# Optimization experiments

Measured on AMD Instinct MI355X. Metric: run time of the kernel, lower is better.

Reference implementation:

```python
import jax, jax.numpy as jnp
import numpy as np

B, L, DM, H, DK, DV, DH = 16, 1024, 512, 8, 64, 64, 2048
FACTOR = 5
EPS = 1e-5


def _ln(x, g, b):
    m = x.mean(-1, keepdims=True)
    v = jnp.mean((x - m) ** 2, axis=-1, keepdims=True)
    return g * (x - m) / jnp.sqrt(v + EPS) + b


def setup_inputs() -> dict:
    key = jax.random.key(0)
    ks = jax.random.split(key, 12)
    w = lambda k, s: jax.random.normal(k, s, jnp.float32) * 0.02
    sample_k = min(FACTOR * int(np.ceil(np.log(L))), L)  # 35
    return {
        "x": jax.random.normal(ks[0], (B, L, DM), jnp.float32),
        "Wq": w(ks[1], (DM, H * DK)), "bq": jnp.zeros((H * DK,), jnp.float32),
        "Wk": w(ks[2], (DM, H * DK)), "bk": jnp.zeros((H * DK,), jnp.float32),
        "Wv": w(ks[3], (DM, H * DV)), "bv": jnp.zeros((H * DV,), jnp.float32),
        "Wo": w(ks[4], (H * DV, DM)), "bo": jnp.zeros((DM,), jnp.float32),
        "g1": jnp.ones((DM,), jnp.float32), "beta1": jnp.zeros((DM,), jnp.float32),
        "W1": w(ks[5], (DM, DH)), "bf1": jnp.zeros((DH,), jnp.float32),
        "W2": w(ks[6], (DH, DM)), "bf2": jnp.zeros((DM,), jnp.float32),
        "g2": jnp.ones((DM,), jnp.float32), "beta2": jnp.zeros((DM,), jnp.float32),
        "index_sample": jax.random.randint(ks[7], (L, sample_k), 0, L),
        "stage": 0,  # eval; mask=False so attn_mask is always False
    }


def _prob_attention(Q, K, V, index_sample):
    # Q,K,V: [B,H,L,D] (Informer ProbAttention, mask_flag=False, eval)
    Bq, Hq, Lq, D = Q.shape
    u = index_sample.shape[1]  # u == U_part since L_Q == L_K
    # sparse sampled scores: K gathered per-query -> [B,H,L,sample_k,D]
    K_sample = K[:, :, index_sample, :]
    QK_sample = jnp.einsum("bhld,bhlsd->bhls", Q, K_sample)
    M = QK_sample.max(-1) - QK_sample.mean(-1)            # [B,H,L] sparsity measure
    _, M_top = jax.lax.top_k(M, u)                         # [B,H,u]
    Q_reduce = jnp.take_along_axis(Q, M_top[..., None], axis=2)  # [B,H,u,D]
    scores = jnp.einsum("bhud,bhld->bhul", Q_reduce, K) / jnp.sqrt(jnp.float32(D))
    attn = jax.nn.softmax(scores, axis=-1)                 # [B,H,u,L]
    # initial context = mean of V over keys, broadcast to all queries
    context = jnp.broadcast_to(V.mean(axis=2, keepdims=True), V.shape)
    bi = jnp.arange(Bq)[:, None, None]
    hi = jnp.arange(Hq)[None, :, None]
    context = context.at[bi, hi, M_top].set(jnp.einsum("bhul,bhld->bhud", attn, V))
    # output_attention=True: uniform 1/L everywhere, true attn at selected queries
    attns = jnp.full((Bq, Hq, Lq, Lq), 1.0 / Lq, dtype=attn.dtype)
    attns = attns.at[bi, hi, M_top].set(attn)
    return context, attns


def reference(x, Wq, bq, Wk, bk, Wv, bv, Wo, bo, g1, beta1, W1, bf1, W2, bf2, g2, beta2, index_sample, stage):
    residual = x
    Q = (x @ Wq + bq).reshape(B, L, H, DK).transpose(0, 2, 1, 3)
    K = (x @ Wk + bk).reshape(B, L, H, DK).transpose(0, 2, 1, 3)
    V = (x @ Wv + bv).reshape(B, L, H, DV).transpose(0, 2, 1, 3)
    ctx, score = _prob_attention(Q, K, V, index_sample)
    ctx = ctx.transpose(0, 2, 1, 3).reshape(B, L, H * DV)
    out = ctx @ Wo + bo
    x1 = _ln(out + residual, g1, beta1)          # dropout = identity (eval)
    ffn = jax.nn.relu(x1 @ W1 + bf1) @ W2 + bf2
    x2 = _ln(ffn + x1, g2, beta2)
    return x2, score
```

## Files before the change

### kernel.cpp

```cpp
#include <hip/hip_runtime.h>
#include <cstdint>
#include <cstddef>

#define Bc 16
#define Lc 1024
#define DMc 512
#define Hc 8
#define DHc 2048
#define Uc 35

typedef __attribute__((ext_vector_type(8))) short bf16x8;
typedef __attribute__((ext_vector_type(4))) float f32x4;

__device__ __forceinline__ ushort f2bf(float f) {
    union { float f; uint32_t u; } v; v.f = f;
    uint32_t r = v.u + 0x7FFF + ((v.u >> 16) & 1);
    return (ushort)(r >> 16);
}
__device__ __forceinline__ float bf2f(ushort u) {
    union { uint32_t i; float f; } v; v.i = ((uint32_t)u) << 16; return v.f;
}

__device__ __forceinline__ void glds16(const ushort* g, ushort* l) {
    __builtin_amdgcn_global_load_lds(
        (__attribute__((address_space(1))) void*)(void*)const_cast<ushort*>(g),
        (__attribute__((address_space(3))) void*)l, 16, 0, 0);
}

template<int MODE>
__global__ __launch_bounds__(256) void gemm_mfma(
    const ushort* __restrict__ A, const ushort* __restrict__ Bt,
    const float* __restrict__ bias, void* __restrict__ out0,
    void* __restrict__ out1, int M, int N, int K, int nxb)
{
    __shared__ ushort As[128 * 64];
    __shared__ ushort Bs[128 * 64];
    const int nwg = gridDim.x;
    int wg = blockIdx.x;
    wg = (wg & 7) * (nwg >> 3) + (wg >> 3);
    const int n0 = (wg % nxb) * 128;
    const int m0 = (wg / nxb) * 128;

    const int tid = threadIdx.x;
    const int lane = tid & 63;
    const int wave = tid >> 6;
    const int wr = wave >> 1, wc = wave & 1;
    const int lrow = lane & 15;
    const int lk = (lane >> 4) * 8;

    f32x4 zero = {0.f, 0.f, 0.f, 0.f};
    f32x4 acc[4][4];
    #pragma unroll
    for (int m = 0; m < 4; ++m)
        #pragma unroll
        for (int n = 0; n < 4; ++n) acc[m][n] = zero;

    const int srow = tid >> 3;
    const int skc = (tid & 7) * 8;
    const int ldsb = (tid & 192) * 8;

    for (int k0 = 0; k0 < K; k0 += 64) {
        #pragma unroll
        for (int r = 0; r < 4; ++r) {
            glds16(A  + (size_t)(m0 + r * 32 + srow) * K + k0 + skc, &As[r * 2048 + ldsb]);
            glds16(Bt + (size_t)(n0 + r * 32 + srow) * K + k0 + skc, &Bs[r * 2048 + ldsb]);
        }
        __syncthreads();
        #pragma unroll
        for (int kk = 0; kk < 2; ++kk) {
            bf16x8 af[4], bv[4];
            #pragma unroll
            for (int m = 0; m < 4; ++m)
                af[m] = *reinterpret_cast<const bf16x8*>(&As[(wr * 64 + m * 16 + lrow) * 64 + kk * 32 + lk]);
            #pragma unroll
            for (int n = 0; n < 4; ++n)
                bv[n] = *reinterpret_cast<const bf16x8*>(&Bs[(wc * 64 + n * 16 + lrow) * 64 + kk * 32 + lk]);
            #pragma unroll
            for (int m = 0; m < 4; ++m)
                #pragma unroll
                for (int n = 0; n < 4; ++n)
                    acc[m][n] = __builtin_amdgcn_mfma_f32_16x16x32_bf16(af[m], bv[n], acc[m][n], 0, 0, 0);
        }
        __syncthreads();
    }

    #pragma unroll
    for (int n = 0; n < 4; ++n) {
        int col = n0 + wc * 64 + n * 16 + lrow;
        float bval = bias[col];
        #pragma unroll
        for (int m = 0; m < 4; ++m) {
            #pragma unroll
            for (int j = 0; j < 4; ++j) {
                int row = m0 + wr * 64 + m * 16 + (lane >> 4) * 4 + j;
                float v = acc[m][n][j] + bval;
                if (MODE == 2) v = fmaxf(v, 0.0f);
                if (MODE == 0)
                    ((float*)out0)[(size_t)row * N + col] = v;
                else if (MODE == 1 || MODE == 2)
                    ((ushort*)out0)[(size_t)row * N + col] = f2bf(v);
                else {
                    if (col < 1024) ((ushort*)out0)[(size_t)row * 1024 + col] = f2bf(v);
                    else            ((float*)out1)[(size_t)row * 512 + (col - 1024)] = v;
                }
            }
        }
    }
}

__device__ __forceinline__ void tr_tile(
    const float* __restrict__ in, ushort* __restrict__ out,
    int K, int N, int bx, int by, float (*t)[33], int tid)
{
    int n0 = bx * 32, k0 = by * 32;
    int tx = tid & 31, ty = tid >> 5;
    #pragma unroll
    for (int dy = 0; dy < 32; dy += 8)
        t[ty + dy][tx] = in[(size_t)(k0 + ty + dy) * N + n0 + tx];
    __syncthreads();
    #pragma unroll
    for (int dy = 0; dy < 32; dy += 8)
        out[(size_t)(n0 + ty + dy) * K + k0 + tx] = f2bf(t[tx][ty + dy]);
}

__global__ __launch_bounds__(256) void prep_kernel(
    const float* __restrict__ x,
    const float* __restrict__ Wq, const float* __restrict__ Wk,
    const float* __restrict__ Wv, const float* __restrict__ Wo,
    const float* __restrict__ W1, const float* __restrict__ W2,
    const float* __restrict__ bq, const float* __restrict__ bk,
    const float* __restrict__ bv,
    ushort* __restrict__ xbf, ushort* __restrict__ Wqkvt,
    ushort* __restrict__ Wot, ushort* __restrict__ W1t,
    ushort* __restrict__ W2t, float* __restrict__ bcat)
{
    __shared__ float t[32][33];
    const int tid = threadIdx.x;
    int bid = blockIdx.x;
    if (bid < 8192) {
        int i = bid * 256 + tid;
        float4 v = reinterpret_cast<const float4*>(x)[i];
        uint32_t lo = (uint32_t)f2bf(v.x) | ((uint32_t)f2bf(v.y) << 16);
        uint32_t hi = (uint32_t)f2bf(v.z) | ((uint32_t)f2bf(v.w) << 16);
        reinterpret_cast<uint2*>(xbf)[i] = make_uint2(lo, hi);
        return;
    }
    bid -= 8192;
    if (bid < 256) { tr_tile(Wq, Wqkvt,              512, 512, bid & 15, bid >> 4, t, tid); return; }
    bid -= 256;
    if (bid < 256) { tr_tile(Wk, Wqkvt + 512 * 512,  512, 512, bid & 15, bid >> 4, t, tid); return; }
    bid -= 256;
    if (bid < 256) { tr_tile(Wv, Wqkvt + 1024 * 512, 512, 512, bid & 15, bid >> 4, t, tid); return; }
    bid -= 256;
    if (bid < 256) { tr_tile(Wo, Wot,                512, 512, bid & 15, bid >> 4, t, tid); return; }
    bid -= 256;
    if (bid < 1024) { tr_tile(W1, W1t,               512, 2048, bid & 63, bid >> 6, t, tid); return; }
    bid -= 1024;
    if (bid < 1024) { tr_tile(W2, W2t,               2048, 512, bid & 15, bid >> 4, t, tid); return; }
    for (int i = tid; i < 1536; i += 256)
        bcat[i] = (i < 512) ? bq[i] : (i < 1024) ? bk[i - 512] : bv[i - 1024];
}

__global__ __launch_bounds__(256) void fill_score_kernel(float* __restrict__ s)
{
    const float iv = 1.0f / (float)Lc;
    float4 v = make_float4(iv, iv, iv, iv);
    size_t i = (size_t)blockIdx.x * 256 + threadIdx.x;
    const size_t nthreads = (size_t)32768 * 256;
    float4* p = reinterpret_cast<float4*>(s);
    #pragma unroll
    for (int c = 0; c < 4; ++c) p[i + c * nthreads] = v;
}

__global__ __launch_bounds__(256) void compute_M_kernel(
    const ushort* __restrict__ QK, const int* __restrict__ idx,
    float* __restrict__ Mout)
{
    __shared__ float qs[4][64];
    const int tid = threadIdx.x;
    const int wid = tid >> 6;
    const int lane = tid & 63;
    const int task = blockIdx.x * 4 + wid;
    const int l = task & (Lc - 1);
    const int bh = task >> 10;
    const int h = bh & (Hc - 1);
    const int b = bh >> 3;

    qs[wid][lane] = bf2f(QK[(size_t)(b * Lc + l) * 1024 + h * 64 + lane]);

    const bool act = lane < Uc;
    int kl = act ? idx[l * Uc + lane] : 0;
    const bf16x8* kr = reinterpret_cast<const bf16x8*>(
        QK + (size_t)(b * Lc + kl) * 1024 + 512 + h * 64);
    float dot = 0.0f;
    if (act) {
        #pragma unroll
        for (int c = 0; c < 8; ++c) {
            bf16x8 kv = kr[c];
            #pragma unroll
            for (int e = 0; e < 8; ++e)
                dot += qs[wid][c * 8 + e] * bf2f((ushort)kv[e]);
        }
    }
    float mx = act ? dot : -INFINITY;
    float sm = act ? dot : 0.0f;
    #pragma unroll
    for (int off = 32; off; off >>= 1) {
        mx = fmaxf(mx, __shfl_xor(mx, off, 64));
        sm += __shfl_xor(sm, off, 64);
    }
    if (lane == 0) Mout[task] = mx - sm * (1.0f / Uc);
}

__global__ __launch_bounds__(256) void topk_kernel(
    const float* __restrict__ Mvals, int* __restrict__ Mtop)
{
    int bh = blockIdx.x;
    __shared__ float vals[Lc];
    __shared__ float rv[256];
    __shared__ int   ri[256];
    int t = threadIdx.x;
    for (int i = t; i < Lc; i += 256)
        vals[i] = Mvals[(size_t)bh * Lc + i];
    __syncthreads();
    for (int j = 0; j < Uc; ++j) {
        float bv = -INFINITY; int bi = Lc;
        for (int i = t; i < Lc; i += 256) {
            float v = vals[i];
            if (v > bv) { bv = v; bi = i; }
        }
        rv[t] = bv; ri[t] = bi;
        __syncthreads();
        for (int s = 128; s; s >>= 1) {
            if (t < s) {
                float v2 = rv[t + s]; int i2 = ri[t + s];
                if (v2 > rv[t] || (v2 == rv[t] && i2 < ri[t])) { rv[t] = v2; ri[t] = i2; }
            }
            __syncthreads();
        }
        if (t == 0) {
            int bidx = ri[0];
            Mtop[bh * Uc + j] = bidx;
            vals[bidx] = -INFINITY;
        }
        __syncthreads();
    }
}

__global__ __launch_bounds__(256) void qk_scores_kernel(
    const ushort* __restrict__ QK, const int* __restrict__ Mtop,
    float* __restrict__ score)
{
    const int bh = blockIdx.x >> 2;
    const int l0 = (blockIdx.x & 3) * 256;
    const int h = bh & (Hc - 1), b = bh >> 3;
    __shared__ int qpos[Uc];
    __shared__ float Qs[Uc][64];
    const int t = threadIdx.x;
    if (t < Uc) qpos[t] = Mtop[bh * Uc + t];
    __syncthreads();
    for (int i = t; i < Uc * 64; i += 256) {
        int j = i >> 6, d = i & 63;
        Qs[j][d] = bf2f(QK[(size_t)(b * Lc + qpos[j]) * 1024 + h * 64 + d]);
    }
    __syncthreads();

    const int l = l0 + t;
    const bf16x8* kr = reinterpret_cast<const bf16x8*>(
        QK + (size_t)(b * Lc + l) * 1024 + 512 + h * 64);
    float acc[Uc] = {};
    #pragma unroll
    for (int c = 0; c < 8; ++c) {
        bf16x8 kv = kr[c];
        float kf[8];
        #pragma unroll
        for (int e = 0; e < 8; ++e) kf[e] = bf2f((ushort)kv[e]);
        #pragma unroll
        for (int j = 0; j < Uc; ++j) {
            float s = 0.0f;
            #pragma unroll
            for (int e = 0; e < 8; ++e) s += Qs[j][c * 8 + e] * kf[e];
            acc[j] += s;
        }
    }
    #pragma unroll
    for (int j = 0; j < Uc; ++j)
        score[((size_t)(bh << 10) + qpos[j]) * Lc + l] = acc[j] * 0.125f;
}

__global__ __launch_bounds__(256) void attn_out_kernel(
    float* __restrict__ score, const float* __restrict__ V,
    const int* __restrict__ Mtop, ushort* __restrict__ ctx)
{
    const int bh = blockIdx.x;
    const int h = bh & (Hc - 1), b = bh >> 3;
    const int t = threadIdx.x;
    const int d = t & 63, part = t >> 6;

    __shared__ int qpos[Uc];
    __shared__ float mz[Uc][2];
    __shared__ float buf[4][Uc][64];
    __shared__ float vmred[4][64];
    __shared__ float vmf[64];

    if (t < Uc) qpos[t] = Mtop[bh * Uc + t];
    __syncthreads();

    for (int j = part; j < Uc; j += 4) {
        const float* row = score + ((size_t)(bh << 10) + qpos[j]) * Lc;
        float v[16];
        float mx = -INFINITY;
        #pragma unroll
        for (int c = 0; c < 16; ++c) { v[c] = row[c * 64 + d]; mx = fmaxf(mx, v[c]); }
        #pragma unroll
        for (int off = 32; off; off >>= 1) mx = fmaxf(mx, __shfl_xor(mx, off, 64));
        float z = 0.0f;
        #pragma unroll
        for (int c = 0; c < 16; ++c) z += expf(v[c] - mx);
        #pragma unroll
        for (int off = 32; off; off >>= 1) z += __shfl_xor(z, off, 64);
        if (d == 0) { mz[j][0] = mx; mz[j][1] = 1.0f / z; }
    }
    __syncthreads();

    float acc[Uc];
    #pragma unroll
    for (int j = 0; j < Uc; ++j) acc[j] = 0.0f;
    float vm = 0.0f;

    for (int c = 0; c < 4; ++c) {
        const int l0 = part * 256 + c * 64;
        #pragma unroll
        for (int j = 0; j < Uc; ++j) {
            size_t off = ((size_t)(bh << 10) + qpos[j]) * Lc + l0 + d;
            float p = expf(score[off] - mz[j][0]) * mz[j][1];
            buf[part][j][d] = p;
            score[off] = p;
        }
        __syncthreads();
        #pragma unroll 4
        for (int li = 0; li < 64; ++li) {
            float v = V[((size_t)(b << 10) + l0 + li) * 512 + h * 64 + d];
            vm += v;
            #pragma unroll
            for (int j = 0; j < Uc; ++j) acc[j] += buf[part][j][li] * v;
        }
        __syncthreads();
    }

    #pragma unroll
    for (int j = 0; j < Uc; ++j) buf[part][j][d] = acc[j];
    vmred[part][d] = vm;
    __syncthreads();
    if (t < 64) vmf[t] = (vmred[0][t] + vmred[1][t] + vmred[2][t] + vmred[3][t]) * (1.0f / Lc);
    __syncthreads();

    const int dcol = (t & 15) * 4;
    ushort4 vmu;
    vmu.x = f2bf(vmf[dcol + 0]); vmu.y = f2bf(vmf[dcol + 1]);
    vmu.z = f2bf(vmf[dcol + 2]); vmu.w = f2bf(vmf[dcol + 3]);
    for (int li = 0; li < 64; ++li) {
        int l = (t >> 4) + li * 16;
        *reinterpret_cast<ushort4*>(ctx + ((size_t)(b << 10) + l) * 512 + h * 64 + dcol) = vmu;
    }
    __syncthreads();

    for (int idx = t; idx < Uc * 64; idx += 256) {
        int j = idx >> 6, d2 = idx & 63;
        float s = buf[0][j][d2] + buf[1][j][d2] + buf[2][j][d2] + buf[3][j][d2];
        ctx[((size_t)(b << 10) + qpos[j]) * 512 + h * 64 + d2] = f2bf(s);
    }
}

template<int A_BF, int B_BF, int OUT_BF>
__global__ __launch_bounds__(256) void ln_kernel(
    const void* __restrict__ a, const void* __restrict__ bsrc,
    const float* __restrict__ g, const float* __restrict__ beta,
    void* __restrict__ y)
{
    const int row = blockIdx.x;
    const int t = threadIdx.x;
    float a0, a1, b0, b1;
    if (A_BF) {
        uint32_t u = ((const uint32_t*)a)[(size_t)row * 256 + t];
        a0 = bf2f((ushort)(u & 0xffff)); a1 = bf2f((ushort)(u >> 16));
    } else {
        float2 f = ((const float2*)a)[(size_t)row * 256 + t];
        a0 = f.x; a1 = f.y;
    }
    if (B_BF) {
        uint32_t u = ((const uint32_t*)bsrc)[(size_t)row * 256 + t];
        b0 = bf2f((ushort)(u & 0xffff)); b1 = bf2f((ushort)(u >> 16));
    } else {
        float2 f = ((const float2*)bsrc)[(size_t)row * 256 + t];
        b0 = f.x; b1 = f.y;
    }
    float v0 = a0 + b0, v1 = a1 + b1;
    __shared__ float red[256];
    red[t] = v0 + v1; __syncthreads();
    for (int s = 128; s; s >>= 1) { if (t < s) red[t] += red[t + s]; __syncthreads(); }
    float mean = red[0] * (1.0f / DMc);
    __syncthreads();
    float d0 = v0 - mean, d1 = v1 - mean;
    red[t] = d0 * d0 + d1 * d1; __syncthreads();
    for (int s = 128; s; s >>= 1) { if (t < s) red[t] += red[t + s]; __syncthreads(); }
    float inv = rsqrtf(red[0] * (1.0f / DMc) + 1e-5f);
    float2 gv = ((const float2*)g)[t];
    float2 bt = ((const float2*)beta)[t];
    float o0 = gv.x * d0 * inv + bt.x;
    float o1 = gv.y * d1 * inv + bt.y;
    if (OUT_BF) {
        uint32_t u = (uint32_t)f2bf(o0) | ((uint32_t)f2bf(o1) << 16);
        ((uint32_t*)y)[(size_t)row * 256 + t] = u;
    } else {
        ((float2*)y)[(size_t)row * 256 + t] = make_float2(o0, o1);
    }
}

extern "C" void kernel_launch(void* const* d_in, const int* in_sizes, int n_in,
                              void* d_out, int out_size, void* d_ws, size_t ws_size,
                              hipStream_t stream)
{
    const float* x     = (const float*)d_in[0];
    const float* Wq    = (const float*)d_in[1];
    const float* bq    = (const float*)d_in[2];
    const float* Wk    = (const float*)d_in[3];
    const float* bk    = (const float*)d_in[4];
    const float* Wv    = (const float*)d_in[5];
    const float* bv    = (const float*)d_in[6];
    const float* Wo    = (const float*)d_in[7];
    const float* bo    = (const float*)d_in[8];
    const float* g1    = (const float*)d_in[9];
    const float* beta1 = (const float*)d_in[10];
    const float* W1    = (const float*)d_in[11];
    const float* bf1   = (const float*)d_in[12];
    const float* W2    = (const float*)d_in[13];
    const float* bf2   = (const float*)d_in[14];
    const float* g2    = (const float*)d_in[15];
    const float* beta2 = (const float*)d_in[16];
    const int* index_sample = (const int*)d_in[17];

    const size_t NTOK = (size_t)Bc * Lc;
    const size_t QKV_SZ = NTOK * DMc;
    const size_t HID_SZ = NTOK * DHc;

    char* p = (char*)d_ws;
    auto alloc = [&](size_t bytes) { char* r = p; p += (bytes + 255) & ~(size_t)255; return r; };
    ushort* QKbf   = (ushort*)alloc(NTOK * 1024 * 2);
    float*  V      = (float*) alloc(QKV_SZ * 4);
    ushort* hidden = (ushort*)alloc(HID_SZ * 2);
    ushort* xbf    = (ushort*)alloc(QKV_SZ * 2);
    ushort* ctxbf  = (ushort*)alloc(QKV_SZ * 2);
    ushort* x1bf   = (ushort*)alloc(QKV_SZ * 2);
    ushort* projbf = (ushort*)alloc(QKV_SZ * 2);
    float*  ffnf   = (float*) alloc(QKV_SZ * 4);
    ushort* Wqkvt  = (ushort*)alloc((size_t)1536 * 512 * 2);
    ushort* Wot    = (ushort*)alloc((size_t)512 * 512 * 2);
    ushort* W1t    = (ushort*)alloc((size_t)512 * 2048 * 2);
    ushort* W2t    = (ushort*)alloc((size_t)512 * 2048 * 2);
    float*  bcat   = (float*) alloc(1536 * 4);
    float*  Mbuf   = (float*) alloc((size_t)Bc * Hc * Lc * 4);
    int*    Mtop   = (int*)   alloc((size_t)Bc * Hc * 64 * 4);

    float* x2_out    = (float*)d_out;
    float* score_out = x2_out + QKV_SZ;

    dim3 blk(256);

    fill_score_kernel<<<32768, blk, 0, stream>>>(score_out);
    prep_kernel<<<8192 + 4 * 256 + 2 * 1024 + 1, blk, 0, stream>>>(
        x, Wq, Wk, Wv, Wo, W1, W2, bq, bk, bv,
        xbf, Wqkvt, Wot, W1t, W2t, bcat);

    gemm_mfma<3><<<12 * 128, blk, 0, stream>>>(
        xbf, Wqkvt, bcat, QKbf, V, (int)NTOK, 1536, 512, 12);

    compute_M_kernel<<<(Bc * Hc * Lc) / 4, blk, 0, stream>>>(QKbf, index_sample, Mbuf);
    topk_kernel<<<Bc * Hc, blk, 0, stream>>>(Mbuf, Mtop);

    qk_scores_kernel<<<Bc * Hc * 4, blk, 0, stream>>>(QKbf, Mtop, score_out);
    attn_out_kernel<<<Bc * Hc, blk, 0, stream>>>(score_out, V, Mtop, ctxbf);

    gemm_mfma<1><<<4 * 128, blk, 0, stream>>>(
        ctxbf, Wot, bo, projbf, nullptr, (int)NTOK, 512, 512, 4);
    ln_kernel<1, 0, 1><<<(int)NTOK, blk, 0, stream>>>(projbf, x, g1, beta1, x1bf);

    gemm_mfma<2><<<16 * 128, blk, 0, stream>>>(
        x1bf, W1t, bf1, hidden, nullptr, (int)NTOK, 2048, 512, 16);
    gemm_mfma<0><<<4 * 128, blk, 0, stream>>>(
        hidden, W2t, bf2, ffnf, nullptr, (int)NTOK, 512, 2048, 4);
    ln_kernel<0, 1, 0><<<(int)NTOK, blk, 0, stream>>>(ffnf, x1bf, g2, beta2, x2_out);
}
```

Measured before the change: 665.0 us.

## Double-buffer GEMM LDS tiles, merge score fill into prep, warp-shuffle top-k

The GEMM now uses two LDS buffers and issues the next K tile's global-to-LDS loads before computing on the current tile, which removes one barrier per iteration and overlaps loads with MFMA. The uniform score fill is merged into the prep kernel to save a launch. Top-k keeps the M values in registers and does the argmax with wave shuffles plus a 4-way final step, replacing the many-barrier LDS tree. Doubling LDS per GEMM block may reduce occupancy.

Result: no change. 667.6 us (+0.4%).

```diff
diff --git a/kernel.cpp b/kernel.cpp
--- a/kernel.cpp
+++ b/kernel.cpp
@@ -33,8 +33,8 @@
     const float* __restrict__ bias, void* __restrict__ out0,
     void* __restrict__ out1, int M, int N, int K, int nxb)
 {
-    __shared__ ushort As[128 * 64];
-    __shared__ ushort Bs[128 * 64];
+    __shared__ ushort As[2][128 * 64];
+    __shared__ ushort Bs[2][128 * 64];
     const int nwg = gridDim.x;
     int wg = blockIdx.x;
     wg = (wg & 7) * (nwg >> 3) + (wg >> 3);
@@ -59,22 +59,29 @@
     const int skc = (tid & 7) * 8;
     const int ldsb = (tid & 192) * 8;
 
-    for (int k0 = 0; k0 < K; k0 += 64) {
+    auto stage = [&](int k0, int bufi) {
         #pragma unroll
         for (int r = 0; r < 4; ++r) {
-            glds16(A  + (size_t)(m0 + r * 32 + srow) * K + k0 + skc, &As[r * 2048 + ldsb]);
-            glds16(Bt + (size_t)(n0 + r * 32 + srow) * K + k0 + skc, &Bs[r * 2048 + ldsb]);
-        }
-        __syncthreads();
+            glds16(A  + (size_t)(m0 + r * 32 + srow) * K + k0 + skc, &As[bufi][r * 2048 + ldsb]);
+            glds16(Bt + (size_t)(n0 + r * 32 + srow) * K + k0 + skc, &Bs[bufi][r * 2048 + ldsb]);
+        }
+    };
+
+    const int nt = K >> 6;
+    stage(0, 0);
+    __syncthreads();
+    int cur = 0;
+    for (int t = 0; t < nt; ++t) {
+        if (t + 1 < nt) stage((t + 1) << 6, cur ^ 1);
         #pragma unroll
         for (int kk = 0; kk < 2; ++kk) {
             bf16x8 af[4], bv[4];
             #pragma unroll
             for (int m = 0; m < 4; ++m)
-                af[m] = *reinterpret_cast<const bf16x8*>(&As[(wr * 64 + m * 16 + lrow) * 64 + kk * 32 + lk]);
+                af[m] = *reinterpret_cast<const bf16x8*>(&As[cur][(wr * 64 + m * 16 + lrow) * 64 + kk * 32 + lk]);
             #pragma unroll
             for (int n = 0; n < 4; ++n)
-                bv[n] = *reinterpret_cast<const bf16x8*>(&Bs[(wc * 64 + n * 16 + lrow) * 64 + kk * 32 + lk]);
+                bv[n] = *reinterpret_cast<const bf16x8*>(&Bs[cur][(wc * 64 + n * 16 + lrow) * 64 + kk * 32 + lk]);
             #pragma unroll
             for (int m = 0; m < 4; ++m)
                 #pragma unroll
@@ -82,6 +89,7 @@
                     acc[m][n] = __builtin_amdgcn_mfma_f32_16x16x32_bf16(af[m], bv[n], acc[m][n], 0, 0, 0);
         }
         __syncthreads();
+        cur ^= 1;
     }
 
     #pragma unroll
@@ -123,6 +131,9 @@
         out[(size_t)(n0 + ty + dy) * K + k0 + tx] = f2bf(t[tx][ty + dy]);
 }
 
+#define PREP_BLKS (8192 + 4 * 256 + 2 * 1024 + 1)
+#define FILL_BLKS 32768
+
 __global__ __launch_bounds__(256) void prep_kernel(
     const float* __restrict__ x,
     const float* __restrict__ Wq, const float* __restrict__ Wk,
@@ -132,7 +143,8 @@
     const float* __restrict__ bv,
     ushort* __restrict__ xbf, ushort* __restrict__ Wqkvt,
     ushort* __restrict__ Wot, ushort* __restrict__ W1t,
-    ushort* __restrict__ W2t, float* __restrict__ bcat)
+    ushort* __restrict__ W2t, float* __restrict__ bcat,
+    float* __restrict__ score_out)
 {
     __shared__ float t[32][33];
     const int tid = threadIdx.x;
@@ -157,17 +169,18 @@
     if (bid < 1024) { tr_tile(W1, W1t,               512, 2048, bid & 63, bid >> 6, t, tid); return; }
     bid -= 1024;
     if (bid < 1024) { tr_tile(W2, W2t,               2048, 512, bid & 15, bid >> 4, t, tid); return; }
-    for (int i = tid; i < 1536; i += 256)
-        bcat[i] = (i < 512) ? bq[i] : (i < 1024) ? bk[i - 512] : bv[i - 1024];
-}
-
-__global__ __launch_bounds__(256) void fill_score_kernel(float* __restrict__ s)
-{
+    bid -= 1024;
+    if (bid < 1) {
+        for (int i = tid; i < 1536; i += 256)
+            bcat[i] = (i < 512) ? bq[i] : (i < 1024) ? bk[i - 512] : bv[i - 1024];
+        return;
+    }
+    bid -= 1;
     const float iv = 1.0f / (float)Lc;
     float4 v = make_float4(iv, iv, iv, iv);
-    size_t i = (size_t)blockIdx.x * 256 + threadIdx.x;
-    const size_t nthreads = (size_t)32768 * 256;
-    float4* p = reinterpret_cast<float4*>(s);
+    size_t i = (size_t)bid * 256 + tid;
+    const size_t nthreads = (size_t)FILL_BLKS * 256;
+    float4* p = reinterpret_cast<float4*>(score_out);
     #pragma unroll
     for (int c = 0; c < 4; ++c) p[i + c * nthreads] = v;
 }
@@ -215,35 +228,41 @@
 __global__ __launch_bounds__(256) void topk_kernel(
     const float* __restrict__ Mvals, int* __restrict__ Mtop)
 {
-    int bh = blockIdx.x;
-    __shared__ float vals[Lc];
-    __shared__ float rv[256];
-    __shared__ int   ri[256];
-    int t = threadIdx.x;
-    for (int i = t; i < Lc; i += 256)
-        vals[i] = Mvals[(size_t)bh * Lc + i];
-    __syncthreads();
+    const int bh = blockIdx.x;
+    const int t = threadIdx.x;
+    const int lane = t & 63, wid = t >> 6;
+    float v[4];
+    #pragma unroll
+    for (int c = 0; c < 4; ++c) v[c] = Mvals[((size_t)bh << 10) + t + 256 * c];
+
+    __shared__ float cv[4];
+    __shared__ int   ci[4];
+    __shared__ int   wini;
+
     for (int j = 0; j < Uc; ++j) {
-        float bv = -INFINITY; int bi = Lc;
-        for (int i = t; i < Lc; i += 256) {
-            float v = vals[i];
-            if (v > bv) { bv = v; bi = i; }
-        }
-        rv[t] = bv; ri[t] = bi;
+        float bv = v[0]; int bi = t;
+        #pragma unroll
+        for (int c = 1; c < 4; ++c)
+            if (v[c] > bv) { bv = v[c]; bi = t + 256 * c; }
+        #pragma unroll
+        for (int off = 32; off; off >>= 1) {
+            float ov = __shfl_xor(bv, off, 64);
+            int   oi = __shfl_xor(bi, off, 64);
+            if (ov > bv || (ov == bv && oi < bi)) { bv = ov; bi = oi; }
+        }
+        if (lane == 0) { cv[wid] = bv; ci[wid] = bi; }
         __syncthreads();
-        for (int s = 128; s; s >>= 1) {
-            if (t < s) {
-                float v2 = rv[t + s]; int i2 = ri[t + s];
-                if (v2 > rv[t] || (v2 == rv[t] && i2 < ri[t])) { rv[t] = v2; ri[t] = i2; }
-            }
-            __syncthreads();
-        }
         if (t == 0) {
-            int bidx = ri[0];
-            Mtop[bh * Uc + j] = bidx;
-            vals[bidx] = -INFINITY;
+            float fv = cv[0]; int fi = ci[0];
+            #pragma unroll
+            for (int w = 1; w < 4; ++w)
+                if (cv[w] > fv || (cv[w] == fv && ci[w] < fi)) { fv = cv[w]; fi = ci[w]; }
+            Mtop[bh * Uc + j] = fi;
+            wini = fi;
         }
         __syncthreads();
+        int wi = wini;
+        if ((wi & 255) == t) v[wi >> 8] = -INFINITY;
     }
 }
 
@@ -467,10 +486,9 @@
 
     dim3 blk(256);
 
-    fill_score_kernel<<<32768, blk, 0, stream>>>(score_out);
-    prep_kernel<<<8192 + 4 * 256 + 2 * 1024 + 1, blk, 0, stream>>>(
+    prep_kernel<<<PREP_BLKS + FILL_BLKS, blk, 0, stream>>>(
         x, Wq, Wk, Wv, Wo, W1, W2, bq, bk, bv,
-        xbf, Wqkvt, Wot, W1t, W2t, bcat);
+        xbf, Wqkvt, Wot, W1t, W2t, bcat, score_out);
 
     gemm_mfma<3><<<12 * 128, blk, 0, stream>>>(
         xbf, Wqkvt, bcat, QKbf, V, (int)NTOK, 1536, 512, 12);
```
